# Kernel tuning notes

Hardware: AMD Instinct MI355X
Metric: run time of the kernel (lower is better)

## Reference

```python
import jax, jax.numpy as jnp
import numpy as np
from jax import lax

LATENT_DIM = 512
UNITS = LATENT_DIM // 2  # per-direction LSTM units (Keras LSTM(latent_dim//2))
FEAT = 512


def _lstm_scan(x, W, U, b):
    """Keras-style LSTM over x: [B, T, F]. Gate order i, f, g(candidate), o.
    Returns (hs [B,T,u], h_last [B,u], c_last [B,u])."""
    B = x.shape[0]
    u = U.shape[0]
    # Precompute input projections for all timesteps (one big GEMM).
    xz = jnp.einsum('btf,fg->btg', x, W) + b  # [B, T, 4u]

    def step(carry, zt):
        h, c = carry
        z = zt + h @ U  # [B, 4u]
        i = jax.nn.sigmoid(z[:, :u])
        f = jax.nn.sigmoid(z[:, u:2 * u])
        g = jnp.tanh(z[:, 2 * u:3 * u])
        o = jax.nn.sigmoid(z[:, 3 * u:])
        c_new = f * c + i * g
        h_new = o * jnp.tanh(c_new)
        return (h_new, c_new), h_new

    init = (jnp.zeros((B, u), x.dtype), jnp.zeros((B, u), x.dtype))
    (h_last, c_last), hs = lax.scan(step, init, jnp.swapaxes(xz, 0, 1))
    return jnp.swapaxes(hs, 0, 1), h_last, c_last


def setup_inputs() -> dict:
    key = jax.random.key(0)
    ks = jax.random.split(key, 7)
    B, T, F, u = 64, 1024, FEAT, UNITS
    s_in = 1.0 / np.sqrt(F)
    s_rec = 1.0 / np.sqrt(u)
    return {
        'x': jax.random.normal(ks[0], (B, T, F), jnp.float32),
        'W_fwd': jax.random.normal(ks[1], (F, 4 * u), jnp.float32) * s_in,
        'U_fwd': jax.random.normal(ks[2], (u, 4 * u), jnp.float32) * s_rec,
        'b_fwd': jnp.zeros((4 * u,), jnp.float32),
        'W_bwd': jax.random.normal(ks[3], (F, 4 * u), jnp.float32) * s_in,
        'U_bwd': jax.random.normal(ks[4], (u, 4 * u), jnp.float32) * s_rec,
        'b_bwd': jnp.zeros((4 * u,), jnp.float32),
    }


def reference(x, W_fwd, U_fwd, b_fwd, W_bwd, U_bwd, b_bwd):
    # Forward direction
    hs_f, h_f, c_f = _lstm_scan(x, W_fwd, U_fwd, b_fwd)
    # Backward direction: process reversed sequence, re-reverse outputs (Keras Bidirectional)
    hs_b, h_b, c_b = _lstm_scan(x[:, ::-1, :], W_bwd, U_bwd, b_bwd)
    hs_b = hs_b[:, ::-1, :]
    enc_out = jnp.concatenate([hs_f, hs_b], axis=-1)  # [B, T, latent]
    h = jnp.concatenate([h_f, h_b], axis=-1)          # [B, latent]
    c = jnp.concatenate([c_f, c_b], axis=-1)          # [B, latent]
    return enc_out, h, c
```

## Files before the change

kernel.cpp:

```cpp
#include <hip/hip_runtime.h>
#include <cstdint>
#include <cstddef>

typedef _Float16 f16x2 __attribute__((ext_vector_type(2)));
typedef _Float16 half4 __attribute__((ext_vector_type(4)));
typedef _Float16 half8 __attribute__((ext_vector_type(8)));
typedef float f32x4 __attribute__((ext_vector_type(4)));

static constexpr int BB = 64;
static constexpr int TT = 1024;
static constexpr int FF = 512;
static constexpr int UU = 256;
static constexpr int NZ = 1024;

static constexpr int LSTM_THREADS = 512;
static constexpr int REG_K2 = 48;
static constexpr int LDS_K2 = 16;
static constexpr size_t LDSU_BYTES = (size_t)LDS_K2 * 512 * 16;
static constexpr size_t PART_BYTES = 256 * 16;
static constexpr size_t HSH_BYTES  = 512;
static constexpr size_t LSTM_SHBYTES = LDSU_BYTES + PART_BYTES + HSH_BYTES;

__device__ __forceinline__ f16x2 bc16(unsigned int v) { return __builtin_bit_cast(f16x2, v); }

__global__ __launch_bounds__(256) void enc_cast_x(
    const float* __restrict__ x, _Float16* __restrict__ x16, int n4)
{
    int stride = gridDim.x * 256;
    for (int i = blockIdx.x * 256 + threadIdx.x; i < n4; i += stride) {
        float4 v = ((const float4*)x)[i];
        half4 o;
        o.x = (_Float16)v.x; o.y = (_Float16)v.y;
        o.z = (_Float16)v.z; o.w = (_Float16)v.w;
        ((half4*)x16)[i] = o;
    }
}

__global__ __launch_bounds__(256) void enc_cast_wt(
    const float* __restrict__ Wf, const float* __restrict__ Wb,
    _Float16* __restrict__ WT)
{
    __shared__ float tile[64][65];
    const int t = threadIdx.x;
    const int k0 = blockIdx.x * 64;
    const int n0 = blockIdx.y * 64;
    const int d = blockIdx.z;
    const float* W = d ? Wb : Wf;
    _Float16* WTd = WT + (size_t)d * NZ * FF;
#pragma unroll
    for (int p = 0; p < 16; ++p) {
        int idx = p * 256 + t;
        int r = idx >> 6, c = idx & 63;
        tile[r][c] = W[(size_t)(k0 + r) * NZ + n0 + c];
    }
    __syncthreads();
#pragma unroll
    for (int p = 0; p < 16; ++p) {
        int idx = p * 256 + t;
        int r = idx >> 6, c = idx & 63;
        WTd[(size_t)(n0 + r) * FF + k0 + c] = (_Float16)tile[c][r];
    }
}

__global__ __launch_bounds__(256) void enc_pack_u16(
    const float* __restrict__ Uf, const float* __restrict__ Ub,
    uint4* __restrict__ Upkr)
{
    int idx = blockIdx.x * 256 + threadIdx.x;
    if (idx >= 2 * 64 * 512) return;
    int d   = idx >> 15;
    int rem = idx & 32767;
    int k2l = rem >> 9;
    int t   = rem & 511;
    int s = t >> 8, j = t & 255;
    int k = s * 128 + 2 * k2l;
    const float* Ud = d ? Ub : Uf;
    unsigned int w[4];
#pragma unroll
    for (int g = 0; g < 4; ++g) {
        f16x2 h;
        h.x = (_Float16)Ud[(size_t)k * NZ + g * 256 + j];
        h.y = (_Float16)Ud[(size_t)(k + 1) * NZ + g * 256 + j];
        w[g] = __builtin_bit_cast(unsigned int, h);
    }
    Upkr[idx] = make_uint4(w[0], w[1], w[2], w[3]);
}

__global__ __launch_bounds__(256) void enc_zero(float* __restrict__ p, int n)
{
    int i = blockIdx.x * 256 + threadIdx.x;
    if (i < n) p[i] = 0.f;
}

__global__ __launch_bounds__(256) void enc_gemm16(
    const _Float16* __restrict__ x16, const _Float16* __restrict__ WT,
    const float* __restrict__ bf, const float* __restrict__ bb,
    _Float16* __restrict__ xz16, int c0, int CT)
{
    __shared__ __align__(16) _Float16 Ash[128][40];
    __shared__ __align__(16) _Float16 Bsh[128][40];

    const int t = threadIdx.x;
    const int r0 = blockIdx.x * 128;
    const int n0 = blockIdx.y * 128;
    const int MperD = BB * CT;
    const int d = r0 / MperD;

    const int srow = t >> 2;
    const int koff = (t & 3) * 8;

    auto xrowptr = [&](int r) -> const _Float16* {
        int rd = r - d * MperD;
        int b = rd / CT;
        int tl = rd - b * CT;
        int tsrc = d ? (TT - 1 - (c0 + tl)) : (c0 + tl);
        return x16 + ((size_t)b * TT + tsrc) * FF;
    };
    const _Float16* ap0 = xrowptr(r0 + srow);
    const _Float16* ap1 = xrowptr(r0 + 64 + srow);
    const _Float16* wp0 = WT + (size_t)(d * NZ + n0 + srow) * FF;
    const _Float16* wp1 = wp0 + (size_t)64 * FF;

    const int lane = t & 63;
    const int w = t >> 6;
    const int wm = w >> 1, wn = w & 1;
    const int l15 = lane & 15;
    const int kq = (lane >> 4) * 8;

    f32x4 acc[4][4];
#pragma unroll
    for (int i = 0; i < 4; ++i)
#pragma unroll
        for (int j = 0; j < 4; ++j) acc[i][j] = (f32x4)0.f;

    for (int ks = 0; ks < FF / 32; ++ks) {
        const int k0 = ks * 32;
        uint4 av0 = *(const uint4*)(ap0 + k0 + koff);
        uint4 av1 = *(const uint4*)(ap1 + k0 + koff);
        uint4 bv0 = *(const uint4*)(wp0 + k0 + koff);
        uint4 bv1 = *(const uint4*)(wp1 + k0 + koff);
        __syncthreads();
        *(uint4*)&Ash[srow][koff]      = av0;
        *(uint4*)&Ash[64 + srow][koff] = av1;
        *(uint4*)&Bsh[srow][koff]      = bv0;
        *(uint4*)&Bsh[64 + srow][koff] = bv1;
        __syncthreads();

        half8 af[4], bfr[4];
#pragma unroll
        for (int mf = 0; mf < 4; ++mf)
            af[mf] = *(const half8*)&Ash[wm * 64 + mf * 16 + l15][kq];
#pragma unroll
        for (int nf = 0; nf < 4; ++nf)
            bfr[nf] = *(const half8*)&Bsh[wn * 64 + nf * 16 + l15][kq];
#pragma unroll
        for (int mf = 0; mf < 4; ++mf)
#pragma unroll
            for (int nf = 0; nf < 4; ++nf)
                acc[mf][nf] = __builtin_amdgcn_mfma_f32_16x16x32_f16(
                    af[mf], bfr[nf], acc[mf][nf], 0, 0, 0);
    }

    const float* bd = d ? bb : bf;
    const int rbase = r0 + wm * 64;
    const int cbase = n0 + wn * 64;
#pragma unroll
    for (int nf = 0; nf < 4; ++nf) {
        const int cc = cbase + nf * 16 + l15;
        const float bia = bd[cc];
#pragma unroll
        for (int mf = 0; mf < 4; ++mf) {
#pragma unroll
            for (int rg = 0; rg < 4; ++rg) {
                int rr = rbase + mf * 16 + (lane >> 4) * 4 + rg;
                xz16[(size_t)rr * NZ + cc] = (_Float16)(acc[mf][nf][rg] + bia);
            }
        }
    }
}

__device__ __forceinline__ float sigm_f(float xv)
{
    return 1.0f / (1.0f + __expf(-xv));
}
__device__ __forceinline__ float tanh_f(float xv)
{
    return 2.0f / (1.0f + __expf(-2.0f * xv)) - 1.0f;
}

__global__ __launch_bounds__(LSTM_THREADS, 2) void enc_lstm_persist(
    const _Float16* __restrict__ xz16, const uint4* __restrict__ Upkr,
    float* __restrict__ hstate, float* __restrict__ cstate,
    float* __restrict__ out, int c0, int CT)
{
    extern __shared__ char smem[];
    uint4*     ldsu = (uint4*)smem;
    float4*    part = (float4*)(smem + LDSU_BYTES);
    _Float16*  hsh  = (_Float16*)(smem + LDSU_BYTES + PART_BYTES);
    uint4*     hshq = (uint4*)hsh;

    const int t = threadIdx.x;
    const int s = t >> 8;
    const int j = t & 255;
    const int bi = blockIdx.x;
    const int d = bi >> 6;
    const int b = bi & 63;

    const uint4* Uq = Upkr + (size_t)d * 64 * 512;
    f16x2 ureg[REG_K2][4];
#pragma unroll
    for (int k2l = 0; k2l < REG_K2; ++k2l) {
        uint4 qv = Uq[(size_t)k2l * 512 + t];
        ureg[k2l][0] = bc16(qv.x);
        ureg[k2l][1] = bc16(qv.y);
        ureg[k2l][2] = bc16(qv.z);
        ureg[k2l][3] = bc16(qv.w);
    }
#pragma unroll
    for (int k2l = REG_K2; k2l < 64; ++k2l)
        ldsu[(size_t)(k2l - REG_K2) * 512 + t] = Uq[(size_t)k2l * 512 + t];

    float c = 0.f;
    if (s == 0) c = cstate[(size_t)(d * BB + b) * UU + j];
    if (t < 256) hsh[t] = (_Float16)hstate[(size_t)(d * BB + b) * UU + t];
    __syncthreads();

    const _Float16* xzrow = xz16 + (size_t)(d * BB + b) * CT * NZ;
    float* outb = out + (size_t)b * TT * (2 * UU) + d * UU;

    float hn = 0.f;
    for (int tl = 0; tl < CT; ++tl) {
        float x0 = 0.f, x1 = 0.f, x2 = 0.f, x3 = 0.f;
        if (s == 0) {
            const _Float16* p = xzrow + (size_t)tl * NZ + j;
            x0 = (float)p[0]; x1 = (float)p[256];
            x2 = (float)p[512]; x3 = (float)p[768];
        }

        float a0 = 0.f, a1 = 0.f, a2 = 0.f, a3 = 0.f;

#pragma unroll
        for (int k2b = 12; k2b < 16; ++k2b) {
            uint4 hq = hshq[s * 16 + k2b];
            f16x2 hw[4] = {bc16(hq.x), bc16(hq.y), bc16(hq.z), bc16(hq.w)};
#pragma unroll
            for (int r = 0; r < 4; ++r) {
                const int k2l = k2b * 4 + r;
                uint4 uq = ldsu[(size_t)(k2l - REG_K2) * 512 + t];
                f16x2 u0 = bc16(uq.x), u1 = bc16(uq.y), u2 = bc16(uq.z), u3 = bc16(uq.w);
                a0 = __builtin_amdgcn_fdot2(hw[r], u0, a0, false);
                a1 = __builtin_amdgcn_fdot2(hw[r], u1, a1, false);
                a2 = __builtin_amdgcn_fdot2(hw[r], u2, a2, false);
                a3 = __builtin_amdgcn_fdot2(hw[r], u3, a3, false);
            }
        }
#pragma unroll
        for (int k2b = 0; k2b < 12; ++k2b) {
            uint4 hq = hshq[s * 16 + k2b];
            f16x2 hw[4] = {bc16(hq.x), bc16(hq.y), bc16(hq.z), bc16(hq.w)};
#pragma unroll
            for (int r = 0; r < 4; ++r) {
                const int k2l = k2b * 4 + r;
                a0 = __builtin_amdgcn_fdot2(hw[r], ureg[k2l][0], a0, false);
                a1 = __builtin_amdgcn_fdot2(hw[r], ureg[k2l][1], a1, false);
                a2 = __builtin_amdgcn_fdot2(hw[r], ureg[k2l][2], a2, false);
                a3 = __builtin_amdgcn_fdot2(hw[r], ureg[k2l][3], a3, false);
            }
        }

        if (s == 1) part[j] = make_float4(a0, a1, a2, a3);
        __syncthreads();

        if (s == 0) {
            float4 pr = part[j];
            float zi = a0 + pr.x + x0;
            float zf = a1 + pr.y + x1;
            float zg = a2 + pr.z + x2;
            float zo = a3 + pr.w + x3;
            float ig = sigm_f(zi), fg = sigm_f(zf), gg = tanh_f(zg), og = sigm_f(zo);
            c = fg * c + ig * gg;
            hn = og * tanh_f(c);
            int tsrc = d ? (TT - 1 - (c0 + tl)) : (c0 + tl);
            outb[(size_t)tsrc * (2 * UU) + j] = hn;
            hsh[j] = (_Float16)hn;
        }
        __syncthreads();
    }

    if (s == 0) {
        hstate[(size_t)(d * BB + b) * UU + j] = hn;
        cstate[(size_t)(d * BB + b) * UU + j] = c;
    }
}

__global__ __launch_bounds__(256) void enc_final(
    const float* __restrict__ hstate, const float* __restrict__ cstate,
    float* __restrict__ out)
{
    int idx = blockIdx.x * 256 + threadIdx.x;
    if (idx >= 2 * BB * UU) return;
    int d = idx / (BB * UU);
    int rem = idx - d * (BB * UU);
    int b = rem / UU;
    int j = rem - b * UU;
    size_t OUT_H = (size_t)BB * TT * (2 * UU);
    size_t HSZ = (size_t)BB * (2 * UU);
    out[OUT_H + (size_t)b * (2 * UU) + d * UU + j] = hstate[idx];
    out[OUT_H + HSZ + (size_t)b * (2 * UU) + d * UU + j] = cstate[idx];
}

extern "C" void kernel_launch(void* const* d_in, const int* in_sizes, int n_in,
                              void* d_out, int out_size, void* d_ws, size_t ws_size,
                              hipStream_t stream)
{
    const float* x  = (const float*)d_in[0];
    const float* Wf = (const float*)d_in[1];
    const float* Uf = (const float*)d_in[2];
    const float* bf = (const float*)d_in[3];
    const float* Wb = (const float*)d_in[4];
    const float* Ub = (const float*)d_in[5];
    const float* bb = (const float*)d_in[6];
    float* out = (float*)d_out;

    const size_t x16_bytes   = (size_t)BB * TT * FF * 2;
    const size_t wt_bytes    = (size_t)2 * NZ * FF * 2;
    const size_t upk_bytes   = (size_t)2 * 64 * 512 * sizeof(uint4);
    const size_t state_bytes = (size_t)2 * BB * UU * sizeof(float);

    int CT = TT;
    while (CT > 8) {
        size_t need = x16_bytes + wt_bytes + upk_bytes + 2 * state_bytes
                    + (size_t)2 * BB * CT * NZ * 2;
        if (need <= ws_size) break;
        CT >>= 1;
    }

    char* wsb = (char*)d_ws;
    _Float16* x16 = (_Float16*)wsb;
    _Float16* WT  = (_Float16*)(wsb + x16_bytes);
    uint4* Upkr   = (uint4*)(wsb + x16_bytes + wt_bytes);
    float* hstate = (float*)(wsb + x16_bytes + wt_bytes + upk_bytes);
    float* cstate = hstate + 2 * BB * UU;
    _Float16* xz16 = (_Float16*)(wsb + x16_bytes + wt_bytes + upk_bytes + 2 * state_bytes);

    (void)hipFuncSetAttribute(reinterpret_cast<const void*>(enc_lstm_persist),
                              hipFuncAttributeMaxDynamicSharedMemorySize,
                              (int)LSTM_SHBYTES);

    enc_cast_x<<<4096, 256, 0, stream>>>(x, x16, BB * TT * FF / 4);
    enc_cast_wt<<<dim3(8, 16, 2), 256, 0, stream>>>(Wf, Wb, WT);
    enc_pack_u16<<<(2 * 64 * 512 + 255) / 256, 256, 0, stream>>>(Uf, Ub, Upkr);
    enc_zero<<<(2 * 2 * BB * UU + 255) / 256, 256, 0, stream>>>(hstate, 2 * 2 * BB * UU);

    for (int c0 = 0; c0 < TT; c0 += CT) {
        dim3 ggrid((2 * BB * CT) / 128, NZ / 128);
        enc_gemm16<<<ggrid, 256, 0, stream>>>(x16, WT, bf, bb, xz16, c0, CT);
        enc_lstm_persist<<<128, LSTM_THREADS, LSTM_SHBYTES, stream>>>(
            xz16, Upkr, hstate, cstate, out, c0, CT);
    }
    enc_final<<<(2 * BB * UU + 255) / 256, 256, 0, stream>>>(hstate, cstate, out);
}
```

Measured before the change: 1.917 ms.

## Split each LSTM sequence across two blocks exchanging h via global flags

Each (direction, batch) recurrence is now handled by two 512-thread blocks, each computing 128 of the 256 hidden units. All recurrent weights fit in registers and the LDS-resident portion is dropped. Partner blocks exchange their half of h every timestep through a double-buffered global buffer, spin-polling on step-tagged relaxed atomics. This doubles the block count to 256 so more CUs work on the serial chain, but it adds a cross-block round trip per step. It also relies on both partner blocks being co-resident, otherwise the spin wait can deadlock.

```diff
diff --git a/kernel.cpp b/kernel.cpp
--- a/kernel.cpp
+++ b/kernel.cpp
@@ -13,15 +13,18 @@
 static constexpr int UU = 256;
 static constexpr int NZ = 1024;
 
-static constexpr int LSTM_THREADS = 512;
-static constexpr int REG_K2 = 48;
-static constexpr int LDS_K2 = 16;
-static constexpr size_t LDSU_BYTES = (size_t)LDS_K2 * 512 * 16;
-static constexpr size_t PART_BYTES = 256 * 16;
-static constexpr size_t HSH_BYTES  = 512;
-static constexpr size_t LSTM_SHBYTES = LDSU_BYTES + PART_BYTES + HSH_BYTES;
+static constexpr size_t LSTM_SHBYTES = 90112;
 
 __device__ __forceinline__ f16x2 bc16(unsigned int v) { return __builtin_bit_cast(f16x2, v); }
+
+__device__ __forceinline__ void st_u32_rlx(unsigned int* p, unsigned int v)
+{
+    __hip_atomic_store(p, v, __ATOMIC_RELAXED, __HIP_MEMORY_SCOPE_AGENT);
+}
+__device__ __forceinline__ unsigned int ld_u32_rlx(const unsigned int* p)
+{
+    return __hip_atomic_load(p, __ATOMIC_RELAXED, __HIP_MEMORY_SCOPE_AGENT);
+}
 
 __global__ __launch_bounds__(256) void enc_cast_x(
     const float* __restrict__ x, _Float16* __restrict__ x16, int n4)
@@ -62,18 +65,16 @@
     }
 }
 
-__global__ __launch_bounds__(256) void enc_pack_u16(
+__global__ __launch_bounds__(256) void enc_pack_u16v2(
     const float* __restrict__ Uf, const float* __restrict__ Ub,
-    uint4* __restrict__ Upkr)
+    uint4* __restrict__ Upkr2)
 {
     int idx = blockIdx.x * 256 + threadIdx.x;
-    if (idx >= 2 * 64 * 512) return;
-    int d   = idx >> 15;
-    int rem = idx & 32767;
-    int k2l = rem >> 9;
-    int t   = rem & 511;
-    int s = t >> 8, j = t & 255;
-    int k = s * 128 + 2 * k2l;
+    if (idx >= 2 * 128 * 256) return;
+    int d  = idx >> 15;
+    int k2 = (idx >> 8) & 127;
+    int j  = idx & 255;
+    int k = 2 * k2;
     const float* Ud = d ? Ub : Uf;
     unsigned int w[4];
 #pragma unroll
@@ -83,7 +84,7 @@
         h.y = (_Float16)Ud[(size_t)(k + 1) * NZ + g * 256 + j];
         w[g] = __builtin_bit_cast(unsigned int, h);
     }
-    Upkr[idx] = make_uint4(w[0], w[1], w[2], w[3]);
+    Upkr2[idx] = make_uint4(w[0], w[1], w[2], w[3]);
 }
 
 __global__ __launch_bounds__(256) void enc_zero(float* __restrict__ p, int n)
@@ -188,108 +189,108 @@
     return 2.0f / (1.0f + __expf(-2.0f * xv)) - 1.0f;
 }
 
-__global__ __launch_bounds__(LSTM_THREADS, 2) void enc_lstm_persist(
-    const _Float16* __restrict__ xz16, const uint4* __restrict__ Upkr,
+__global__ __launch_bounds__(512, 2) void enc_lstm_split(
+    const _Float16* __restrict__ xz16, const uint4* __restrict__ Upkr2,
     float* __restrict__ hstate, float* __restrict__ cstate,
+    unsigned int* __restrict__ hbuf,
     float* __restrict__ out, int c0, int CT)
 {
-    extern __shared__ char smem[];
-    uint4*     ldsu = (uint4*)smem;
-    float4*    part = (float4*)(smem + LDSU_BYTES);
-    _Float16*  hsh  = (_Float16*)(smem + LDSU_BYTES + PART_BYTES);
-    uint4*     hshq = (uint4*)hsh;
-
-    const int t = threadIdx.x;
-    const int s = t >> 8;
-    const int j = t & 255;
-    const int bi = blockIdx.x;
-    const int d = bi >> 6;
-    const int b = bi & 63;
-
-    const uint4* Uq = Upkr + (size_t)d * 64 * 512;
-    f16x2 ureg[REG_K2][4];
-#pragma unroll
-    for (int k2l = 0; k2l < REG_K2; ++k2l) {
-        uint4 qv = Uq[(size_t)k2l * 512 + t];
-        ureg[k2l][0] = bc16(qv.x);
-        ureg[k2l][1] = bc16(qv.y);
-        ureg[k2l][2] = bc16(qv.z);
-        ureg[k2l][3] = bc16(qv.w);
-    }
-#pragma unroll
-    for (int k2l = REG_K2; k2l < 64; ++k2l)
-        ldsu[(size_t)(k2l - REG_K2) * 512 + t] = Uq[(size_t)k2l * 512 + t];
-
-    float c = 0.f;
-    if (s == 0) c = cstate[(size_t)(d * BB + b) * UU + j];
-    if (t < 256) hsh[t] = (_Float16)hstate[(size_t)(d * BB + b) * UU + t];
+    extern __shared__ char smem2[];
+    float4*    parts = (float4*)smem2;
+    _Float16*  hsh   = (_Float16*)(smem2 + 6144);
+    uint4*     hshq  = (uint4*)hsh;
+
+    const int t  = threadIdx.x;
+    const int s  = t >> 7;
+    const int jl = t & 127;
+    const int beta = blockIdx.x;
+    const int jh = (beta >> 3) & 1;
+    const int c  = ((beta >> 4) << 3) | (beta & 7);
+    const int d  = c >> 6;
+    const int b  = c & 63;
+    const int j  = jh * 128 + jl;
+    const int partner = beta ^ 8;
+
+    const uint4* Uq = Upkr2 + ((size_t)d * 128 + s * 32) * 256 + j;
+    f16x2 ureg[32][4];
+#pragma unroll
+    for (int m = 0; m < 32; ++m) {
+        uint4 qv = Uq[(size_t)m * 256];
+        ureg[m][0] = bc16(qv.x);
+        ureg[m][1] = bc16(qv.y);
+        ureg[m][2] = bc16(qv.z);
+        ureg[m][3] = bc16(qv.w);
+    }
+
+    float cr = 0.f, hn = 0.f;
+    if (s == 0) cr = cstate[(size_t)c * UU + j];
+    if (t < 256) hsh[t] = (_Float16)hstate[(size_t)c * UU + t];
     __syncthreads();
 
-    const _Float16* xzrow = xz16 + (size_t)(d * BB + b) * CT * NZ;
+    const _Float16* xzrow = xz16 + (size_t)c * CT * NZ;
     float* outb = out + (size_t)b * TT * (2 * UU) + d * UU;
 
-    float hn = 0.f;
     for (int tl = 0; tl < CT; ++tl) {
+        const int step = c0 + tl + 1;
+
         float x0 = 0.f, x1 = 0.f, x2 = 0.f, x3 = 0.f;
         if (s == 0) {
             const _Float16* p = xzrow + (size_t)tl * NZ + j;
-            x0 = (float)p[0]; x1 = (float)p[256];
+            x0 = (float)p[0];   x1 = (float)p[256];
             x2 = (float)p[512]; x3 = (float)p[768];
         }
 
         float a0 = 0.f, a1 = 0.f, a2 = 0.f, a3 = 0.f;
-
-#pragma unroll
-        for (int k2b = 12; k2b < 16; ++k2b) {
-            uint4 hq = hshq[s * 16 + k2b];
+#pragma unroll
+        for (int r = 0; r < 8; ++r) {
+            uint4 hq = hshq[s * 8 + r];
             f16x2 hw[4] = {bc16(hq.x), bc16(hq.y), bc16(hq.z), bc16(hq.w)};
 #pragma unroll
-            for (int r = 0; r < 4; ++r) {
-                const int k2l = k2b * 4 + r;
-                uint4 uq = ldsu[(size_t)(k2l - REG_K2) * 512 + t];
-                f16x2 u0 = bc16(uq.x), u1 = bc16(uq.y), u2 = bc16(uq.z), u3 = bc16(uq.w);
-                a0 = __builtin_amdgcn_fdot2(hw[r], u0, a0, false);
-                a1 = __builtin_amdgcn_fdot2(hw[r], u1, a1, false);
-                a2 = __builtin_amdgcn_fdot2(hw[r], u2, a2, false);
-                a3 = __builtin_amdgcn_fdot2(hw[r], u3, a3, false);
+            for (int q = 0; q < 4; ++q) {
+                const int m = r * 4 + q;
+                a0 = __builtin_amdgcn_fdot2(hw[q], ureg[m][0], a0, false);
+                a1 = __builtin_amdgcn_fdot2(hw[q], ureg[m][1], a1, false);
+                a2 = __builtin_amdgcn_fdot2(hw[q], ureg[m][2], a2, false);
+                a3 = __builtin_amdgcn_fdot2(hw[q], ureg[m][3], a3, false);
             }
         }
-#pragma unroll
-        for (int k2b = 0; k2b < 12; ++k2b) {
-            uint4 hq = hshq[s * 16 + k2b];
-            f16x2 hw[4] = {bc16(hq.x), bc16(hq.y), bc16(hq.z), bc16(hq.w)};
-#pragma unroll
-            for (int r = 0; r < 4; ++r) {
-                const int k2l = k2b * 4 + r;
-                a0 = __builtin_amdgcn_fdot2(hw[r], ureg[k2l][0], a0, false);
-                a1 = __builtin_amdgcn_fdot2(hw[r], ureg[k2l][1], a1, false);
-                a2 = __builtin_amdgcn_fdot2(hw[r], ureg[k2l][2], a2, false);
-                a3 = __builtin_amdgcn_fdot2(hw[r], ureg[k2l][3], a3, false);
-            }
-        }
-
-        if (s == 1) part[j] = make_float4(a0, a1, a2, a3);
+
+        if (s) parts[(s - 1) * 128 + jl] = make_float4(a0, a1, a2, a3);
         __syncthreads();
 
         if (s == 0) {
-            float4 pr = part[j];
-            float zi = a0 + pr.x + x0;
-            float zf = a1 + pr.y + x1;
-            float zg = a2 + pr.z + x2;
-            float zo = a3 + pr.w + x3;
+            float4 p1 = parts[jl], p2 = parts[128 + jl], p3 = parts[256 + jl];
+            float zi = a0 + p1.x + p2.x + p3.x + x0;
+            float zf = a1 + p1.y + p2.y + p3.y + x1;
+            float zg = a2 + p1.z + p2.z + p3.z + x2;
+            float zo = a3 + p1.w + p2.w + p3.w + x3;
             float ig = sigm_f(zi), fg = sigm_f(zf), gg = tanh_f(zg), og = sigm_f(zo);
-            c = fg * c + ig * gg;
-            hn = og * tanh_f(c);
+            cr = fg * cr + ig * gg;
+            hn = og * tanh_f(cr);
+            _Float16 h16 = (_Float16)hn;
+            st_u32_rlx(&hbuf[((size_t)(step & 1) * 256 + beta) * 128 + jl],
+                       ((unsigned int)step << 16)
+                       | (unsigned int)__builtin_bit_cast(unsigned short, h16));
+            hsh[j] = h16;
             int tsrc = d ? (TT - 1 - (c0 + tl)) : (c0 + tl);
             outb[(size_t)tsrc * (2 * UU) + j] = hn;
-            hsh[j] = (_Float16)hn;
+        }
+        if (s == 1) {
+            const unsigned int* p =
+                &hbuf[((size_t)(step & 1) * 256 + partner) * 128 + jl];
+            unsigned int v;
+            do {
+                v = ld_u32_rlx(p);
+            } while ((v >> 16) != (unsigned int)step);
+            hsh[(1 - jh) * 128 + jl] =
+                __builtin_bit_cast(_Float16, (unsigned short)(v & 0xffffu));
         }
         __syncthreads();
     }
 
     if (s == 0) {
-        hstate[(size_t)(d * BB + b) * UU + j] = hn;
-        cstate[(size_t)(d * BB + b) * UU + j] = c;
+        hstate[(size_t)c * UU + j] = hn;
+        cstate[(size_t)c * UU + j] = cr;
     }
 }
 
@@ -324,13 +325,15 @@
 
     const size_t x16_bytes   = (size_t)BB * TT * FF * 2;
     const size_t wt_bytes    = (size_t)2 * NZ * FF * 2;
-    const size_t upk_bytes   = (size_t)2 * 64 * 512 * sizeof(uint4);
+    const size_t upk_bytes   = (size_t)2 * 128 * 256 * sizeof(uint4);
     const size_t state_bytes = (size_t)2 * BB * UU * sizeof(float);
+    const size_t hbuf_bytes  = (size_t)2 * 256 * 128 * 4;
+    const size_t fixed = x16_bytes + wt_bytes + upk_bytes + 2 * state_bytes
+                       + hbuf_bytes;
 
     int CT = TT;
     while (CT > 8) {
-        size_t need = x16_bytes + wt_bytes + upk_bytes + 2 * state_bytes
-                    + (size_t)2 * BB * CT * NZ * 2;
+        size_t need = fixed + (size_t)2 * BB * CT * NZ * 2;
         if (need <= ws_size) break;
         CT >>= 1;
     }
@@ -338,25 +341,27 @@
     char* wsb = (char*)d_ws;
     _Float16* x16 = (_Float16*)wsb;
     _Float16* WT  = (_Float16*)(wsb + x16_bytes);
-    uint4* Upkr   = (uint4*)(wsb + x16_bytes + wt_bytes);
+    uint4* Upkr2  = (uint4*)(wsb + x16_bytes + wt_bytes);
     float* hstate = (float*)(wsb + x16_bytes + wt_bytes + upk_bytes);
     float* cstate = hstate + 2 * BB * UU;
-    _Float16* xz16 = (_Float16*)(wsb + x16_bytes + wt_bytes + upk_bytes + 2 * state_bytes);
-
-    (void)hipFuncSetAttribute(reinterpret_cast<const void*>(enc_lstm_persist),
+    unsigned int* hbuf = (unsigned int*)(wsb + x16_bytes + wt_bytes + upk_bytes
+                                         + 2 * state_bytes);
+    _Float16* xz16 = (_Float16*)(wsb + fixed);
+
+    (void)hipFuncSetAttribute(reinterpret_cast<const void*>(enc_lstm_split),
                               hipFuncAttributeMaxDynamicSharedMemorySize,
                               (int)LSTM_SHBYTES);
 
     enc_cast_x<<<4096, 256, 0, stream>>>(x, x16, BB * TT * FF / 4);
     enc_cast_wt<<<dim3(8, 16, 2), 256, 0, stream>>>(Wf, Wb, WT);
-    enc_pack_u16<<<(2 * 64 * 512 + 255) / 256, 256, 0, stream>>>(Uf, Ub, Upkr);
+    enc_pack_u16v2<<<(2 * 128 * 256 + 255) / 256, 256, 0, stream>>>(Uf, Ub, Upkr2);
     enc_zero<<<(2 * 2 * BB * UU + 255) / 256, 256, 0, stream>>>(hstate, 2 * 2 * BB * UU);
 
     for (int c0 = 0; c0 < TT; c0 += CT) {
         dim3 ggrid((2 * BB * CT) / 128, NZ / 128);
         enc_gemm16<<<ggrid, 256, 0, stream>>>(x16, WT, bf, bb, xz16, c0, CT);
-        enc_lstm_persist<<<128, LSTM_THREADS, LSTM_SHBYTES, stream>>>(
-            xz16, Upkr, hstate, cstate, out, c0, CT);
+        enc_lstm_split<<<256, 512, LSTM_SHBYTES, stream>>>(
+            xz16, Upkr2, hstate, cstate, hbuf, out, c0, CT);
     }
     enc_final<<<(2 * BB * UU + 255) / 256, 256, 0, stream>>>(hstate, cstate, out);
 }
```

Result: faster. 1.878 ms (-2.0%).
